# Kernel tuning notes

Measured on AMD Instinct MI355X. Metric: run time of the kernel, lower is better.

## Reference

```python
import jax, jax.numpy as jnp
import numpy as np

NUM_HEADS = 16
EMBED_DIM = 1024
HEAD_DIM = EMBED_DIM // NUM_HEADS
REG_LEN = 2048
SUM_LEN = 64
BSZ = 2
REL_DIM = 64
NUM_REL_EMB = 64
MAX_SUMMARY = 64
SCALE = HEAD_DIM ** -0.5


def _ln(x, g, b, eps=1e-5):
    m = jnp.mean(x, axis=-1, keepdims=True)
    v = jnp.mean((x - m) ** 2, axis=-1, keepdims=True)
    return (x - m) * jax.lax.rsqrt(v + eps) * g + b


def setup_inputs() -> dict:
    key = jax.random.key(0)
    ks = jax.random.split(key, 16)
    inp = {}
    inp['reg_x'] = jax.random.normal(ks[0], (REG_LEN, BSZ, EMBED_DIM), jnp.float32)
    inp['sum_token_ids'] = jax.random.randint(ks[1], (BSZ, SUM_LEN), 0, MAX_SUMMARY + 1)
    inp['rel_idx'] = jax.random.randint(ks[2], (BSZ, SUM_LEN + REG_LEN, REG_LEN), 0, NUM_REL_EMB)
    inp['sum_len'] = SUM_LEN
    inp['reg_len'] = REG_LEN
    emb = jax.random.normal(ks[3], (MAX_SUMMARY + 1, EMBED_DIM), jnp.float32) * 0.02
    inp['emb_sum'] = emb.at[0].set(0.0)  # padding_idx = 0
    inp['rel_emb0'] = jax.random.normal(ks[4], (NUM_REL_EMB, REL_DIM), jnp.float32) * 0.02

    def lin(k, din, dout):
        return jax.random.normal(k, (din, dout), jnp.float32) * (1.0 / np.sqrt(din))

    inp['Wq'] = lin(ks[5], EMBED_DIM, EMBED_DIM); inp['bq'] = jnp.zeros((EMBED_DIM,), jnp.float32)
    inp['Wk'] = lin(ks[6], EMBED_DIM, EMBED_DIM); inp['bk'] = jnp.zeros((EMBED_DIM,), jnp.float32)
    inp['Wv'] = lin(ks[7], EMBED_DIM, EMBED_DIM); inp['bv'] = jnp.zeros((EMBED_DIM,), jnp.float32)
    inp['Wr0'] = lin(ks[8], REL_DIM, EMBED_DIM); inp['br0'] = jnp.zeros((EMBED_DIM,), jnp.float32)
    inp['Wk2'] = lin(ks[9], HEAD_DIM, HEAD_DIM); inp['bk2'] = jnp.zeros((HEAD_DIM,), jnp.float32)
    inp['Wv2'] = lin(ks[10], HEAD_DIM, HEAD_DIM); inp['bv2'] = jnp.zeros((HEAD_DIM,), jnp.float32)
    inp['Wo'] = lin(ks[11], EMBED_DIM, EMBED_DIM); inp['bo'] = jnp.zeros((EMBED_DIM,), jnp.float32)
    for name in ['ln_k', 'ln_v', 'ln_k2', 'ln_v2']:
        inp[name + '_g'] = jnp.ones((HEAD_DIM,), jnp.float32)
        inp[name + '_b'] = jnp.zeros((HEAD_DIM,), jnp.float32)
    return inp


def reference(reg_x, sum_token_ids, rel_idx, sum_len, reg_len, emb_sum, rel_emb0,
              Wq, bq, Wk, bk, Wv, bv, Wr0, br0, Wk2, bk2, Wv2, bv2, Wo, bo,
              ln_k_g, ln_k_b, ln_v_g, ln_v_b, ln_k2_g, ln_k2_b, ln_v2_g, ln_v2_b):
    R, B, E = reg_x.shape  # reg_len, bsz, embed_dim
    H, D = NUM_HEADS, HEAD_DIM
    S = sum_token_ids.shape[1]

    # regular K/V projections + per-head LayerNorm
    reg_k = _ln((reg_x @ Wk + bk).reshape(R, B, H, D), ln_k_g, ln_k_b)
    reg_v = _ln((reg_x @ Wv + bv).reshape(R, B, H, D), ln_v_g, ln_v_b)

    # relation-type embedding projection -> [Rrel, H, D]
    r0 = (rel_emb0 @ Wr0 + br0).reshape(NUM_REL_EMB, H, D)

    # --- stage 1: summary tokens attend over regular tokens ---
    sum_x = emb_sum[sum_token_ids.T]                     # [S, B, E]
    sum_q = sum_x.reshape(S, B, H, D) * SCALE
    scores_sum = jnp.einsum('sbhd,kbhd->bhsk', sum_q, reg_k)   # [B,H,S,R]
    qr_sum = jnp.einsum('sbhd,Zhd->bhsZ', sum_q, r0)           # [B,H,S,Rrel]
    idx_sum = rel_idx[:, :S]                                   # [B,S,R]
    scores_sum = scores_sum + jnp.take_along_axis(qr_sum, idx_sum[:, None, :, :], axis=-1)
    w_sum = jax.nn.softmax(scores_sum, axis=-1)
    sum_x2 = jnp.einsum('bhsk,kbhd->sbhd', w_sum, reg_v)       # [S,B,H,D]

    sum_k2 = _ln(sum_x2 @ Wk2 + bk2, ln_k2_g, ln_k2_b)
    sum_v2 = _ln(sum_x2 @ Wv2 + bv2, ln_v2_g, ln_v2_b)

    # --- stage 2: regular tokens attend over [summary ; regular] keys ---
    reg_q = (reg_x @ Wq + bq).reshape(R, B, H, D) * SCALE
    scores_rs = jnp.einsum('qbhd,sbhd->bhqs', reg_q, sum_k2)   # [B,H,R,S]
    scores_rr = jnp.einsum('qbhd,kbhd->bhqk', reg_q, reg_k)    # [B,H,R,R]
    qr_reg = jnp.einsum('qbhd,Zhd->bhqZ', reg_q, r0)
    idx_reg = rel_idx[:, S:]                                   # [B,R,R]
    scores_rr = scores_rr + jnp.take_along_axis(qr_reg, idx_reg[:, None, :, :], axis=-1)
    scores = jnp.concatenate([scores_rs, scores_rr], axis=-1)  # [B,H,R,S+R]
    w = jax.nn.softmax(scores, axis=-1)
    v_all = jnp.concatenate([sum_v2, reg_v], axis=0)           # [S+R,B,H,D]
    attn_out = jnp.einsum('bhqk,kbhd->qbhd', w, v_all).reshape(R, B, E)
    reg_x2 = attn_out @ Wo + bo
    return reg_x2
```

## Files before the change

### kernel.cpp

```cpp
#include <hip/hip_runtime.h>
#include <cstdint>
#include <cstddef>

#define NH   16
#define HD   64
#define RLEN 2048
#define BSZ  2
#define SLEN 64
#define NZ   64
#define ED   1024
#define KTOT 2112
#define NSPLIT 16

#define QSCALE 0.18033688011112042f

typedef __bf16 bf16_t;
typedef bf16_t bf16x8 __attribute__((ext_vector_type(8)));
typedef bf16_t bf16x4 __attribute__((ext_vector_type(4)));
typedef float  f32x4  __attribute__((ext_vector_type(4)));

__device__ __forceinline__ f32x4 mfma16(bf16x8 a, bf16x8 b, f32x4 c) {
    return __builtin_amdgcn_mfma_f32_16x16x32_bf16(a, b, c, 0, 0, 0);
}

__device__ __forceinline__ void dma16(const void* g, void* l) {
    __builtin_amdgcn_global_load_lds(
        (const __attribute__((address_space(1))) unsigned int*)g,
        (__attribute__((address_space(3))) unsigned int*)l, 16, 0, 0);
}


template<int BM>
__global__ __launch_bounds__(256) void gemm_fast(
    const bf16_t* __restrict__ A, const bf16_t* __restrict__ Bt,
    const float* __restrict__ b0, const float* __restrict__ b1,
    const float* __restrict__ b2,
    bf16_t* __restrict__ oq, float* __restrict__ o1, float* __restrict__ o2,
    int M, int K, int N, int mode)
{
    constexpr int MT = BM / 64;
    __shared__ __align__(16) bf16_t As[BM * 64];
    __shared__ __align__(16) bf16_t Bs[128 * 64];

    const int t = threadIdx.x;
    const int wave = t >> 6, lane = t & 63;
    const int quad = lane >> 4, l15 = lane & 15;
    const int rsub = lane >> 3, gq = lane & 7;
    const int m0 = blockIdx.y * BM, n0 = blockIdx.x * 128;

    f32x4 acc[MT][8];
#pragma unroll
    for (int i = 0; i < MT; i++)
#pragma unroll
        for (int j = 0; j < 8; j++) acc[i][j] = (f32x4){0.f, 0.f, 0.f, 0.f};

    for (int k0 = 0; k0 < K; k0 += 64) {
#pragma unroll
        for (int j = 0; j < BM / 32; j++) {
            int row = wave * (BM / 4) + j * 8 + rsub;
            const bf16_t* g = A + (size_t)(m0 + row) * K + k0 + ((gq ^ (row & 7)) * 8);
            dma16(g, As + (wave * (BM / 4) + j * 8) * 64);
        }
#pragma unroll
        for (int j = 0; j < 4; j++) {
            int row = wave * 32 + j * 8 + rsub;
            const bf16_t* g = Bt + (size_t)(n0 + row) * K + k0 + ((gq ^ (row & 7)) * 8);
            dma16(g, Bs + (wave * 32 + j * 8) * 64);
        }
        __syncthreads();

#pragma unroll
        for (int kk = 0; kk < 2; kk++) {
            const int pg = ((kk * 4 + quad) ^ (l15 & 7)) * 8;
            bf16x8 af[MT], bf[8];
#pragma unroll
            for (int mt = 0; mt < MT; mt++)
                af[mt] = *(const bf16x8*)(As + (wave * (BM / 4) + mt * 16 + l15) * 64 + pg);
#pragma unroll
            for (int nt = 0; nt < 8; nt++)
                bf[nt] = *(const bf16x8*)(Bs + (nt * 16 + l15) * 64 + pg);
#pragma unroll
            for (int mt = 0; mt < MT; mt++)
#pragma unroll
                for (int nt = 0; nt < 8; nt++)
                    acc[mt][nt] = mfma16(af[mt], bf[nt], acc[mt][nt]);
        }
        __syncthreads();
    }

#pragma unroll
    for (int mt = 0; mt < MT; mt++)
#pragma unroll
        for (int nt = 0; nt < 8; nt++)
#pragma unroll
            for (int reg = 0; reg < 4; reg++) {
                int m = m0 + wave * (BM / 4) + mt * 16 + quad * 4 + reg;
                int n = n0 + nt * 16 + l15;
                if (mode == 0) {
                    o1[(size_t)m * N + n] = acc[mt][nt][reg] + b0[n];
                } else {
                    int seg = n >> 10, nl = n & 1023;
                    const float* bias = (seg == 0) ? b0 : (seg == 1) ? b1 : b2;
                    float c = acc[mt][nt][reg] + bias[nl];
                    int h = nl >> 6, d = nl & 63;
                    int r = m >> 1, bb = m & 1;
                    size_t off = (((size_t)bb * NH + h) * RLEN + r) * HD + d;
                    if (seg == 0)      oq[off] = (bf16_t)(c * QSCALE);
                    else if (seg == 1) o1[off] = c;
                    else               o2[off] = c;
                }
            }
}

__global__ __launch_bounds__(256) void gemm_mfma(
    const bf16_t* __restrict__ A, const bf16_t* __restrict__ Bt,
    const float* __restrict__ bias, float* __restrict__ outf,
    int M, int K, int N, int Rr)
{
    constexpr int LDA = 40;
    __shared__ __align__(16) bf16_t As[64 * LDA];
    __shared__ __align__(16) bf16_t Bs[128 * LDA];

    const int t = threadIdx.x;
    const int wave = t >> 6, lane = t & 63;
    const int quad = lane >> 4, l15 = lane & 15;
    const int wrow = wave >> 1, wcol = wave & 1;
    const int m0 = blockIdx.y * 64, n0 = blockIdx.x * 128;

    f32x4 acc[2][4];
#pragma unroll
    for (int i = 0; i < 2; i++)
#pragma unroll
        for (int j = 0; j < 4; j++) acc[i][j] = (f32x4){0.f, 0.f, 0.f, 0.f};

    const int srow = t >> 2, sseg = (t & 3) * 8;

    for (int k0 = 0; k0 < K; k0 += 32) {
        bf16x8 av  = *(const bf16x8*)(A  + (size_t)(m0 + srow) * K + k0 + sseg);
        bf16x8 bv0 = *(const bf16x8*)(Bt + (size_t)(n0 + srow) * K + k0 + sseg);
        bf16x8 bv1 = *(const bf16x8*)(Bt + (size_t)(n0 + 64 + srow) * K + k0 + sseg);
        __syncthreads();
        *(bf16x8*)(As + srow * LDA + sseg)        = av;
        *(bf16x8*)(Bs + srow * LDA + sseg)        = bv0;
        *(bf16x8*)(Bs + (64 + srow) * LDA + sseg) = bv1;
        __syncthreads();

        bf16x8 af[2], bf[4];
#pragma unroll
        for (int mt = 0; mt < 2; mt++)
            af[mt] = *(const bf16x8*)(As + (wrow * 32 + mt * 16 + l15) * LDA + quad * 8);
#pragma unroll
        for (int nt = 0; nt < 4; nt++)
            bf[nt] = *(const bf16x8*)(Bs + (wcol * 64 + nt * 16 + l15) * LDA + quad * 8);
#pragma unroll
        for (int mt = 0; mt < 2; mt++)
#pragma unroll
            for (int nt = 0; nt < 4; nt++)
                acc[mt][nt] = mfma16(af[mt], bf[nt], acc[mt][nt]);
    }

#pragma unroll
    for (int mt = 0; mt < 2; mt++)
#pragma unroll
        for (int nt = 0; nt < 4; nt++)
#pragma unroll
            for (int reg = 0; reg < 4; reg++) {
                int m = m0 + wrow * 32 + mt * 16 + quad * 4 + reg;
                int n = n0 + wcol * 64 + nt * 16 + l15;
                if (m >= M) continue;
                float c = acc[mt][nt][reg] + bias[n];
                int h = n >> 6, d = n & 63;
                outf[(((size_t)h) * Rr + m) * HD + d] = c;
            }
}

__global__ __launch_bounds__(256) void ln_k_frag(
    const float* __restrict__ x, const float* __restrict__ g, const float* __restrict__ b,
    bf16_t* __restrict__ kfm)
{
    int row  = blockIdx.x * 4 + (threadIdx.x >> 6);
    int lane = threadIdx.x & 63;
    float v = x[(size_t)row * HD + lane];
    float s1 = v, s2 = v * v;
#pragma unroll
    for (int o = 32; o > 0; o >>= 1) {
        s1 += __shfl_xor(s1, o);
        s2 += __shfl_xor(s2, o);
    }
    float mean = s1 * (1.f / 64.f);
    float var  = s2 * (1.f / 64.f) - mean * mean;
    float y = (v - mean) * rsqrtf(var + 1e-5f) * g[lane] + b[lane];
    int bh = row >> 11, r = row & 2047, d = lane;
    int rt = r & 63;
    size_t off = (size_t)bh * 131072 + (size_t)(r >> 6) * 4096 +
        (size_t)((((rt & 3) * 2 + (d >> 5)) * 64 + ((d >> 3) & 3) * 16 + (rt >> 2)) * 8 + (d & 7));
    kfm[off] = (bf16_t)y;
}

__global__ __launch_bounds__(256) void lnv_frag(
    const float* __restrict__ v, const float* __restrict__ g,
    const float* __restrict__ b, bf16_t* __restrict__ vfm)
{
    __shared__ float tile[64][65];
    const int bh = blockIdx.y, tidx = blockIdx.x;
    const int t = threadIdx.x;
    const int wave = t >> 6, lane = t & 63;

#pragma unroll
    for (int i = 0; i < 16; i++) {
        int rl = wave * 16 + i;
        float x = v[((size_t)bh * RLEN + tidx * 64 + rl) * HD + lane];
        float s1 = x, s2 = x * x;
#pragma unroll
        for (int o = 32; o > 0; o >>= 1) {
            s1 += __shfl_xor(s1, o);
            s2 += __shfl_xor(s2, o);
        }
        float mean = s1 * (1.f / 64.f);
        float var  = s2 * (1.f / 64.f) - mean * mean;
        tile[rl][lane] = (x - mean) * rsqrtf(var + 1e-5f) * g[lane] + b[lane];
    }
    __syncthreads();
    int d = t >> 2, rs = (t & 3) * 16;
    bf16x8 o0, o1;
#pragma unroll
    for (int j = 0; j < 8; j++) {
        o0[j] = (bf16_t)tile[rs + j][d];
        o1[j] = (bf16_t)tile[rs + 8 + j][d];
    }
    size_t base = (size_t)bh * 131072;
    size_t off0 = base + (size_t)((((tidx * 4 + (d >> 4)) * 2 + (rs >> 5)) * 64
                  + ((rs >> 3) & 3) * 16 + (d & 15)) * 8);
    int rs2 = rs + 8;
    size_t off1 = base + (size_t)((((tidx * 4 + (d >> 4)) * 2 + (rs2 >> 5)) * 64
                  + ((rs2 >> 3) & 3) * 16 + (d & 15)) * 8);
    *(bf16x8*)(vfm + off0) = o0;
    *(bf16x8*)(vfm + off1) = o1;
}

__global__ __launch_bounds__(256) void cvt_bf16(
    const float* __restrict__ src, bf16_t* __restrict__ dst, int n)
{
    int i = (blockIdx.x * 256 + threadIdx.x) * 4;
    if (i < n) {
        float4 v = *(const float4*)(src + i);
        bf16x4 o;
        o[0] = (bf16_t)v.x; o[1] = (bf16_t)v.y; o[2] = (bf16_t)v.z; o[3] = (bf16_t)v.w;
        *(bf16x4*)(dst + i) = o;
    }
}

__global__ __launch_bounds__(256) void prep_batch(
    const float* __restrict__ Wq, const float* __restrict__ Wk,
    const float* __restrict__ Wv, const float* __restrict__ Wo,
    const float* __restrict__ Wr0,
    bf16_t* __restrict__ wqt, bf16_t* __restrict__ wkt,
    bf16_t* __restrict__ wvt, bf16_t* __restrict__ wot,
    bf16_t* __restrict__ wr0t,
    const float* __restrict__ emb, const int* __restrict__ ids,
    bf16_t* __restrict__ sum_q,
    const float* __restrict__ rel_emb0, bf16_t* __restrict__ re0b)
{
    const int bid = blockIdx.x;
    const int t = threadIdx.x;

    if (bid >= 1168) {
        int i = ((bid - 1168) * 256 + t) * 4;
        float4 v = *(const float4*)(rel_emb0 + i);
        bf16x4 o;
        o[0] = (bf16_t)v.x; o[1] = (bf16_t)v.y; o[2] = (bf16_t)v.z; o[3] = (bf16_t)v.w;
        *(bf16x4*)(re0b + i) = o;
        return;
    }
    if (bid >= 1040) {
        int sb = bid - 1040;
        int s = sb >> 1, b = sb & 1;
        int id = ids[b * SLEN + s];
        const float* src = emb + (size_t)id * ED;
        for (int e = t; e < ED; e += 256) {
            int h = e >> 6, d = e & 63;
            sum_q[(((size_t)b * NH + h) * SLEN + s) * HD + d] = (bf16_t)(src[e] * QSCALE);
        }
        return;
    }

    __shared__ float tile[64][65];
    const float* src; bf16_t* dst; int R, C, r0, c0;
    if (bid < 1024) {
        int sel = bid >> 8, local = bid & 255;
        src = (sel == 0) ? Wq : (sel == 1) ? Wk : (sel == 2) ? Wv : Wo;
        dst = (sel == 0) ? wqt : (sel == 1) ? wkt : (sel == 2) ? wvt : wot;
        R = ED; C = ED; r0 = (local >> 4) * 64; c0 = (local & 15) * 64;
    } else {
        src = Wr0; dst = wr0t; R = NZ; C = ED; r0 = 0; c0 = (bid - 1024) * 64;
    }
#pragma unroll
    for (int i = 0; i < 4; i++) {
        int idx = t + i * 256;
        int r = idx >> 4, c = (idx & 15) * 4;
        float4 vv = *(const float4*)(src + (size_t)(r0 + r) * C + c0 + c);
        tile[r][c] = vv.x; tile[r][c + 1] = vv.y; tile[r][c + 2] = vv.z; tile[r][c + 3] = vv.w;
    }
    __syncthreads();
    int cc = t >> 2, rs = (t & 3) * 16;
    bf16x8 o0, o1;
#pragma unroll
    for (int j = 0; j < 8; j++) {
        o0[j] = (bf16_t)tile[rs + j][cc];
        o1[j] = (bf16_t)tile[rs + 8 + j][cc];
    }
    *(bf16x8*)(dst + (size_t)(c0 + cc) * R + r0 + rs) = o0;
    *(bf16x8*)(dst + (size_t)(c0 + cc) * R + r0 + rs + 8) = o1;
}

template<int MT>
__device__ __forceinline__ void attn_tile(
    const bf16_t* __restrict__ ktn, const bf16_t* __restrict__ vtn, int koffn,
    const int* __restrict__ relbase, bool userel,
    const float* __restrict__ qrsw, bf16_t* __restrict__ Psw,
    const bf16x8 (&qf)[MT][2],
    bf16x8 (&kf)[4][2], bf16x8 (&vf)[4][2], int4 (&crel)[MT][4],
    f32x4 (&O)[MT][4], float (&l_i)[MT][4],
    int quad, int l15, int lane)
{
    f32x4 S[MT][4];
#pragma unroll
    for (int mt = 0; mt < MT; mt++)
#pragma unroll
        for (int nt = 0; nt < 4; nt++) {
            f32x4 acc = (f32x4){0.f, 0.f, 0.f, 0.f};
            acc = mfma16(qf[mt][0], kf[nt][0], acc);
            acc = mfma16(qf[mt][1], kf[nt][1], acc);
            S[mt][nt] = acc;
        }

#pragma unroll
    for (int nt = 0; nt < 4; nt++)
#pragma unroll
        for (int kb = 0; kb < 2; kb++)
            kf[nt][kb] = *(const bf16x8*)(ktn + ((nt * 2 + kb) * 64 + lane) * 8);

    if (userel) {
#pragma unroll
        for (int mt = 0; mt < MT; mt++)
#pragma unroll
            for (int reg = 0; reg < 4; reg++) {
                const float* qr = qrsw + (mt * 16 + quad * 4 + reg) * 64;
                int4 c = crel[mt][reg];
                S[mt][0][reg] += qr[c.x];
                S[mt][1][reg] += qr[c.y];
                S[mt][2][reg] += qr[c.z];
                S[mt][3][reg] += qr[c.w];
            }
    }

#pragma unroll
    for (int mt = 0; mt < MT; mt++)
#pragma unroll
        for (int reg = 0; reg < 4; reg++)
            crel[mt][reg] = *(const int4*)(relbase + (size_t)(mt * 16 + reg) * RLEN + koffn);

#pragma unroll
    for (int mt = 0; mt < MT; mt++)
#pragma unroll
        for (int nt = 0; nt < 4; nt++)
#pragma unroll
            for (int reg = 0; reg < 4; reg++)
                S[mt][nt][reg] = exp2f(S[mt][nt][reg]);

    bf16x8 ones;
#pragma unroll
    for (int j = 0; j < 8; j++) ones[j] = (bf16_t)1.0f;

#pragma unroll
    for (int mt = 0; mt < MT; mt++)
#pragma unroll
        for (int reg = 0; reg < 4; reg++) {
            bf16x4 pv;
            pv[0] = (bf16_t)S[mt][0][reg]; pv[1] = (bf16_t)S[mt][1][reg];
            pv[2] = (bf16_t)S[mt][2][reg]; pv[3] = (bf16_t)S[mt][3][reg];
            *(bf16x4*)(Psw + (mt * 16 + quad * 4 + reg) * 72 + 4 * l15) = pv;
        }

#pragma unroll
    for (int mt = 0; mt < MT; mt++) {
        bf16x8 pf0 = *(const bf16x8*)(Psw + (mt * 16 + l15) * 72 + quad * 8);
        bf16x8 pf1 = *(const bf16x8*)(Psw + (mt * 16 + l15) * 72 + 32 + quad * 8);
        f32x4 ls = (f32x4){0.f, 0.f, 0.f, 0.f};
        ls = mfma16(pf0, ones, ls);
        ls = mfma16(pf1, ones, ls);
#pragma unroll
        for (int nt = 0; nt < 4; nt++) {
            O[mt][nt] = mfma16(pf0, vf[nt][0], O[mt][nt]);
            O[mt][nt] = mfma16(pf1, vf[nt][1], O[mt][nt]);
        }
#pragma unroll
        for (int reg = 0; reg < 4; reg++) l_i[mt][reg] += ls[reg];
    }

#pragma unroll
    for (int nt = 0; nt < 4; nt++)
#pragma unroll
        for (int kb = 0; kb < 2; kb++)
            vf[nt][kb] = *(const bf16x8*)(vtn + ((nt * 2 + kb) * 64 + lane) * 8);
}

__device__ __forceinline__ void load_kv(
    bf16x8 (&kf)[4][2], bf16x8 (&vf)[4][2],
    const bf16_t* __restrict__ kt, const bf16_t* __restrict__ vt, int lane)
{
#pragma unroll
    for (int nt = 0; nt < 4; nt++)
#pragma unroll
        for (int kb = 0; kb < 2; kb++) {
            kf[nt][kb] = *(const bf16x8*)(kt + ((nt * 2 + kb) * 64 + lane) * 8);
            vf[nt][kb] = *(const bf16x8*)(vt + ((nt * 2 + kb) * 64 + lane) * 8);
        }
}

template<int MT>
__device__ __forceinline__ void build_qr(
    const float* __restrict__ r0, int h, const bf16x8 (&qf)[MT][2],
    float* __restrict__ qrsw, int quad, int l15)
{
#pragma unroll
    for (int nt = 0; nt < 4; nt++) {
        const float* rp = r0 + ((size_t)h * NZ + l15 + 16 * nt) * HD + quad * 8;
        float4 a0 = *(const float4*)(rp);
        float4 a1 = *(const float4*)(rp + 4);
        bf16x8 bf0;
        bf0[0] = (bf16_t)a0.x; bf0[1] = (bf16_t)a0.y; bf0[2] = (bf16_t)a0.z; bf0[3] = (bf16_t)a0.w;
        bf0[4] = (bf16_t)a1.x; bf0[5] = (bf16_t)a1.y; bf0[6] = (bf16_t)a1.z; bf0[7] = (bf16_t)a1.w;
        float4 b0 = *(const float4*)(rp + 32);
        float4 b1 = *(const float4*)(rp + 36);
        bf16x8 bf1;
        bf1[0] = (bf16_t)b0.x; bf1[1] = (bf16_t)b0.y; bf1[2] = (bf16_t)b0.z; bf1[3] = (bf16_t)b0.w;
        bf1[4] = (bf16_t)b1.x; bf1[5] = (bf16_t)b1.y; bf1[6] = (bf16_t)b1.z; bf1[7] = (bf16_t)b1.w;
#pragma unroll
        for (int mt = 0; mt < MT; mt++) {
            f32x4 qa = (f32x4){0.f, 0.f, 0.f, 0.f};
            qa = mfma16(qf[mt][0], bf0, qa);
            qa = mfma16(qf[mt][1], bf1, qa);
#pragma unroll
            for (int reg = 0; reg < 4; reg++)
                qrsw[(mt * 16 + quad * 4 + reg) * 64 + l15 + 16 * nt] = qa[reg];
        }
    }
}

__global__ __launch_bounds__(256) void sum_attn_split(
    const bf16_t* __restrict__ Qb,
    const bf16_t* __restrict__ kfm, const bf16_t* __restrict__ vfm,
    const float*  __restrict__ r0,
    const int*    __restrict__ rel_idx,
    float* __restrict__ po, float* __restrict__ pl)
{
    constexpr int TPS = 32 / NSPLIT;
    const int bh = blockIdx.x;
    const int split = blockIdx.y;
    const int b = bh >> 4, h = bh & 15;
    const int t = threadIdx.x;
    const int wave = t >> 6, lane = t & 63;
    const int quad = lane >> 4, l15 = lane & 15;

    __shared__ __align__(16) bf16_t Ps[4][16 * 72];
    __shared__ float qrs[4][16 * 64];

    bf16x8 qf[1][2];
    const bf16_t* Qrow = Qb + ((size_t)bh * SLEN + wave * 16 + l15) * HD;
    qf[0][0] = *(const bf16x8*)(Qrow + quad * 8);
    qf[0][1] = *(const bf16x8*)(Qrow + 32 + quad * 8);

    const int* relbase = rel_idx + ((size_t)b * KTOT + wave * 16 + quad * 4) * RLEN + 4 * l15;
    const bf16_t* kbase = kfm + (size_t)bh * 131072 + (size_t)(split * TPS) * 4096;
    const bf16_t* vbase = vfm + (size_t)bh * 131072 + (size_t)(split * TPS) * 4096;

    bf16x8 kf[4][2], vf[4][2];
    int4 crel[1][4];
    load_kv(kf, vf, kbase, vbase, lane);
#pragma unroll
    for (int reg = 0; reg < 4; reg++)
        crel[0][reg] = *(const int4*)(relbase + (size_t)reg * RLEN + split * TPS * 64);

    build_qr<1>(r0, h, qf, qrs[wave], quad, l15);

    f32x4 O[1][4];
    float l_i[1][4];
#pragma unroll
    for (int nt = 0; nt < 4; nt++) O[0][nt] = (f32x4){0.f, 0.f, 0.f, 0.f};
#pragma unroll
    for (int r = 0; r < 4; r++) l_i[0][r] = 0.f;

    for (int i = 0; i < TPS; i++) {
        const int nx = (i < TPS - 1) ? i + 1 : i;
        attn_tile<1>(kbase + (size_t)nx * 4096, vbase + (size_t)nx * 4096,
                     (split * TPS + nx) * 64, relbase, true,
                     qrs[wave], Ps[wave], qf, kf, vf, crel,
                     O, l_i, quad, l15, lane);
    }

    const size_t pslot = (size_t)bh * NSPLIT + split;
#pragma unroll
    for (int nt = 0; nt < 4; nt++)
#pragma unroll
        for (int reg = 0; reg < 4; reg++) {
            int sq = wave * 16 + quad * 4 + reg;
            po[(pslot * SLEN + sq) * HD + l15 + 16 * nt] = O[0][nt][reg];
        }
#pragma unroll
    for (int reg = 0; reg < 4; reg++) {
        int sq = wave * 16 + quad * 4 + reg;
        if (l15 == 0) pl[pslot * SLEN + sq] = l_i[0][reg];
    }
}

__global__ __launch_bounds__(64) void k2v2_fused(
    const float* __restrict__ po, const float* __restrict__ pl,
    const float* __restrict__ Wk2, const float* __restrict__ bk2,
    const float* __restrict__ Wv2, const float* __restrict__ bv2,
    const float* __restrict__ gk, const float* __restrict__ bk,
    const float* __restrict__ gv, const float* __restrict__ bv,
    bf16_t* __restrict__ k2fm, bf16_t* __restrict__ v2fm)
{
    int row = blockIdx.x;
    int d = threadIdx.x;
    int bh = row >> 6, s = row & 63;

    float L = 0.f, acc = 0.f;
#pragma unroll
    for (int j = 0; j < NSPLIT; j++) {
        L += pl[((size_t)bh * NSPLIT + j) * SLEN + s];
        acc += po[(((size_t)bh * NSPLIT + j) * SLEN + s) * HD + d];
    }
    __shared__ float xs[64];
    xs[d] = acc / L;
    __syncthreads();

#pragma unroll
    for (int which = 0; which < 2; which++) {
        const float* W  = which ? Wv2 : Wk2;
        const float* bi = which ? bv2 : bk2;
        const float* g  = which ? gv : gk;
        const float* bb = which ? bv : bk;
        float a = bi[d];
#pragma unroll
        for (int j = 0; j < 64; j++) a += xs[j] * W[j * HD + d];
        float s1 = a, s2 = a * a;
#pragma unroll
        for (int o = 32; o > 0; o >>= 1) {
            s1 += __shfl_xor(s1, o);
            s2 += __shfl_xor(s2, o);
        }
        float mean = s1 * (1.f / 64.f);
        float var  = s2 * (1.f / 64.f) - mean * mean;
        float y = (a - mean) * rsqrtf(var + 1e-5f) * g[d] + bb[d];
        if (which == 0) {
            size_t off = (size_t)bh * 4096 +
                (size_t)((((s & 3) * 2 + (d >> 5)) * 64
                          + ((d >> 3) & 3) * 16 + (s >> 2)) * 8 + (d & 7));
            k2fm[off] = (bf16_t)y;
        } else {
            size_t off = (size_t)bh * 4096 +
                (size_t)((((d >> 4) * 2 + (s >> 5)) * 64
                          + ((s >> 3) & 3) * 16 + (d & 15)) * 8 + (s & 7));
            v2fm[off] = (bf16_t)y;
        }
    }
}

__global__ __launch_bounds__(256) void reg_attn_mfma(
    const bf16_t* __restrict__ Qb,
    const bf16_t* __restrict__ kfm, const bf16_t* __restrict__ vfm,
    const bf16_t* __restrict__ k2fm, const bf16_t* __restrict__ v2fm,
    const float*  __restrict__ r0,
    const int*    __restrict__ rel_idx,
    bf16_t* __restrict__ attn_out)
{
    const int bid = blockIdx.x;
    const int bh = (bid & 7) * 4 + ((bid >> 3) & 3);
    const int qt = bid >> 5;
    const int b = bh >> 4, h = bh & 15;
    const int q0 = qt * 128;

    const int t = threadIdx.x;
    const int wave = t >> 6, lane = t & 63;
    const int quad = lane >> 4, l15 = lane & 15;

    __shared__ __align__(16) bf16_t Ps[4][32 * 72];
    __shared__ float qrs[4][32 * 64];

    bf16x8 qf[2][2];
#pragma unroll
    for (int mt = 0; mt < 2; mt++) {
        const bf16_t* Qrow = Qb + ((size_t)bh * RLEN + q0 + wave * 32 + mt * 16 + l15) * HD;
        qf[mt][0] = *(const bf16x8*)(Qrow + quad * 8);
        qf[mt][1] = *(const bf16x8*)(Qrow + 32 + quad * 8);
    }

    bf16x8 kf[4][2], vf[4][2];
    int4 crel[2][4];
    load_kv(kf, vf, k2fm + (size_t)bh * 4096, v2fm + (size_t)bh * 4096, lane);

    build_qr<2>(r0, h, qf, qrs[wave], quad, l15);

    f32x4 O[2][4];
    float l_i[2][4];
#pragma unroll
    for (int mt = 0; mt < 2; mt++)
#pragma unroll
        for (int nt = 0; nt < 4; nt++) O[mt][nt] = (f32x4){0.f, 0.f, 0.f, 0.f};
#pragma unroll
    for (int mt = 0; mt < 2; mt++)
#pragma unroll
        for (int r = 0; r < 4; r++) l_i[mt][r] = 0.f;

    const int* relbase = rel_idx +
        ((size_t)b * KTOT + SLEN + q0 + wave * 32 + quad * 4) * RLEN + 4 * l15;

    const bf16_t* kt = kfm + (size_t)bh * 131072;
    const bf16_t* vt = vfm + (size_t)bh * 131072;

    attn_tile<2>(kt, vt, 0, relbase, false, qrs[wave], Ps[wave], qf,
                 kf, vf, crel, O, l_i, quad, l15, lane);

    for (int tile = 0; tile < 32; tile++) {
        const int nx = (tile < 31) ? tile + 1 : tile;
        attn_tile<2>(kt + (size_t)nx * 4096, vt + (size_t)nx * 4096, nx * 64,
                     relbase, true, qrs[wave], Ps[wave], qf,
                     kf, vf, crel, O, l_i, quad, l15, lane);
    }

#pragma unroll
    for (int mt = 0; mt < 2; mt++) {
        float linv[4];
#pragma unroll
        for (int reg = 0; reg < 4; reg++) linv[reg] = 1.0f / l_i[mt][reg];
#pragma unroll
        for (int nt = 0; nt < 4; nt++)
#pragma unroll
            for (int reg = 0; reg < 4; reg++) {
                int q = q0 + wave * 32 + mt * 16 + quad * 4 + reg;
                attn_out[((size_t)q * BSZ + b) * ED + h * HD + l15 + 16 * nt] =
                    (bf16_t)(O[mt][nt][reg] * linv[reg]);
            }
    }
}

extern "C" void kernel_launch(void* const* d_in, const int* in_sizes, int n_in,
                              void* d_out, int out_size, void* d_ws, size_t ws_size,
                              hipStream_t stream)
{
    const float* reg_x    = (const float*)d_in[0];
    const int*   sum_ids  = (const int*)d_in[1];
    const int*   rel_idx  = (const int*)d_in[2];
    const float* emb_sum  = (const float*)d_in[5];
    const float* rel_emb0 = (const float*)d_in[6];
    const float* Wq = (const float*)d_in[7];
    const float* bq = (const float*)d_in[8];
    const float* Wk = (const float*)d_in[9];
    const float* bk = (const float*)d_in[10];
    const float* Wv = (const float*)d_in[11];
    const float* bv = (const float*)d_in[12];
    const float* Wr0 = (const float*)d_in[13];
    const float* br0 = (const float*)d_in[14];
    const float* Wk2 = (const float*)d_in[15];
    const float* bk2 = (const float*)d_in[16];
    const float* Wv2 = (const float*)d_in[17];
    const float* bv2 = (const float*)d_in[18];
    const float* Wo  = (const float*)d_in[19];
    const float* bo  = (const float*)d_in[20];
    const float* ln_k_g  = (const float*)d_in[21];
    const float* ln_k_b  = (const float*)d_in[22];
    const float* ln_v_g  = (const float*)d_in[23];
    const float* ln_v_b  = (const float*)d_in[24];
    const float* ln_k2_g = (const float*)d_in[25];
    const float* ln_k2_b = (const float*)d_in[26];
    const float* ln_v2_g = (const float*)d_in[27];
    const float* ln_v2_b = (const float*)d_in[28];

    const size_t QKV = (size_t)BSZ * NH * RLEN * HD;
    const size_t SUM = (size_t)BSZ * NH * SLEN * HD;

    float* ws  = (float*)d_ws;
    float* k   = ws;
    float* v   = k + QKV;
    float* r0  = v + QKV;

    bf16_t* xb   = (bf16_t*)(r0 + (size_t)NH * NZ * HD);
    bf16_t* qb   = xb + QKV;
    bf16_t* kfm  = qb + QKV;
    bf16_t* vfm  = kfm + QKV;
    bf16_t* sqb  = vfm + QKV;
    bf16_t* k2fm = sqb + SUM;
    bf16_t* v2fm = k2fm + SUM;
    bf16_t* wqt  = v2fm + SUM;
    bf16_t* wkt  = wqt + (size_t)ED * ED;
    bf16_t* wvt  = wkt + (size_t)ED * ED;
    bf16_t* wot  = wvt + (size_t)ED * ED;
    bf16_t* wr0t = wot + (size_t)ED * ED;
    bf16_t* re0b = wr0t + (size_t)ED * NZ;
    bf16_t* aob  = (bf16_t*)k;
    float*  po   = v;
    float*  pl   = po + (size_t)BSZ * NH * NSPLIT * SLEN * HD;

    const int M = RLEN * BSZ;

    cvt_bf16<<<(int)(QKV / 1024), 256, 0, stream>>>(reg_x, xb, (int)QKV);
    prep_batch<<<1172, 256, 0, stream>>>(Wq, Wk, Wv, Wo, Wr0,
                                         wqt, wkt, wvt, wot, wr0t,
                                         emb_sum, sum_ids, sqb, rel_emb0, re0b);

    gemm_fast<128><<<dim3(3 * ED / 128, M / 128), 256, 0, stream>>>(
        xb, wqt, bq, bk, bv, qb, k, v, M, ED, 3 * ED, 1);

    ln_k_frag<<<(BSZ * NH * RLEN) / 4, 256, 0, stream>>>(k, ln_k_g, ln_k_b, kfm);
    lnv_frag<<<dim3(RLEN / 64, BSZ * NH), 256, 0, stream>>>(v, ln_v_g, ln_v_b, vfm);

    gemm_mfma<<<dim3(ED / 128, 1), 256, 0, stream>>>(re0b, wr0t, br0, r0, NZ, NZ, ED, NZ);

    sum_attn_split<<<dim3(BSZ * NH, NSPLIT), 256, 0, stream>>>(sqb, kfm, vfm, r0, rel_idx, po, pl);

    k2v2_fused<<<BSZ * NH * SLEN, 64, 0, stream>>>(po, pl, Wk2, bk2, Wv2, bv2,
                                                   ln_k2_g, ln_k2_b, ln_v2_g, ln_v2_b,
                                                   k2fm, v2fm);

    reg_attn_mfma<<<512, 256, 0, stream>>>(qb, kfm, vfm, k2fm, v2fm, r0, rel_idx, aob);

    gemm_fast<64><<<dim3(ED / 128, M / 64), 256, 0, stream>>>(
        aob, wot, bo, nullptr, nullptr, nullptr, (float*)d_out, nullptr, M, ED, ED, 0);
}
```

Before: 370.7 us.

## Fuse K/V LayerNorm and fragment layout into QKV GEMM epilogue

```diff
diff --git a/kernel.cpp b/kernel.cpp
--- a/kernel.cpp
+++ b/kernel.cpp
@@ -35,12 +35,16 @@
     const bf16_t* __restrict__ A, const bf16_t* __restrict__ Bt,
     const float* __restrict__ b0, const float* __restrict__ b1,
     const float* __restrict__ b2,
-    bf16_t* __restrict__ oq, float* __restrict__ o1, float* __restrict__ o2,
+    const float* __restrict__ gk_, const float* __restrict__ bk_,
+    const float* __restrict__ gv_, const float* __restrict__ bv_,
+    bf16_t* __restrict__ oq, float* __restrict__ o1,
+    bf16_t* __restrict__ okf, bf16_t* __restrict__ ovf,
     int M, int K, int N, int mode)
 {
     constexpr int MT = BM / 64;
     __shared__ __align__(16) bf16_t As[BM * 64];
     __shared__ __align__(16) bf16_t Bs[128 * 64];
+    __shared__ __align__(16) bf16_t trs[64][66];
 
     const int t = threadIdx.x;
     const int wave = t >> 6, lane = t & 63;
@@ -88,28 +92,137 @@
         __syncthreads();
     }
 
-#pragma unroll
-    for (int mt = 0; mt < MT; mt++)
-#pragma unroll
-        for (int nt = 0; nt < 8; nt++)
+    if (mode == 0) {
+#pragma unroll
+        for (int mt = 0; mt < MT; mt++)
+#pragma unroll
+            for (int nt = 0; nt < 8; nt++)
+#pragma unroll
+                for (int reg = 0; reg < 4; reg++) {
+                    int m = m0 + wave * (BM / 4) + mt * 16 + quad * 4 + reg;
+                    int n = n0 + nt * 16 + l15;
+                    o1[(size_t)m * N + n] = acc[mt][nt][reg] + b0[n];
+                }
+        return;
+    }
+
+    const int seg = n0 >> 10;
+    if (seg == 0) {
+#pragma unroll
+        for (int mt = 0; mt < MT; mt++)
+#pragma unroll
+            for (int nt = 0; nt < 8; nt++)
+#pragma unroll
+                for (int reg = 0; reg < 4; reg++) {
+                    int m = m0 + wave * (BM / 4) + mt * 16 + quad * 4 + reg;
+                    int n = n0 + nt * 16 + l15;
+                    float c = acc[mt][nt][reg] + b0[n];
+                    int h = n >> 6, d = n & 63;
+                    int r = m >> 1, bb2 = m & 1;
+                    size_t off = (((size_t)bb2 * NH + h) * RLEN + r) * HD + d;
+                    oq[off] = (bf16_t)(c * QSCALE);
+                }
+        return;
+    }
+
+    const int nl0 = n0 & 1023, h0 = nl0 >> 6;
+    const float* bias = (seg == 1) ? b1 : b2;
+    const float* lg = (seg == 1) ? gk_ : gv_;
+    const float* lb = (seg == 1) ? bk_ : bv_;
+    float gj[4], bj[4], bsv[2][4];
+#pragma unroll
+    for (int j = 0; j < 4; j++) { gj[j] = lg[j * 16 + l15]; bj[j] = lb[j * 16 + l15]; }
+#pragma unroll
+    for (int h2 = 0; h2 < 2; h2++)
+#pragma unroll
+        for (int j = 0; j < 4; j++)
+            bsv[h2][j] = bias[nl0 + (h2 * 4 + j) * 16 + l15];
+
+    if (seg == 1) {
+#pragma unroll
+        for (int mt = 0; mt < MT; mt++)
 #pragma unroll
             for (int reg = 0; reg < 4; reg++) {
                 int m = m0 + wave * (BM / 4) + mt * 16 + quad * 4 + reg;
-                int n = n0 + nt * 16 + l15;
-                if (mode == 0) {
-                    o1[(size_t)m * N + n] = acc[mt][nt][reg] + b0[n];
-                } else {
-                    int seg = n >> 10, nl = n & 1023;
-                    const float* bias = (seg == 0) ? b0 : (seg == 1) ? b1 : b2;
-                    float c = acc[mt][nt][reg] + bias[nl];
-                    int h = nl >> 6, d = nl & 63;
-                    int r = m >> 1, bb = m & 1;
-                    size_t off = (((size_t)bb * NH + h) * RLEN + r) * HD + d;
-                    if (seg == 0)      oq[off] = (bf16_t)(c * QSCALE);
-                    else if (seg == 1) o1[off] = c;
-                    else               o2[off] = c;
+                int r = m >> 1, bb2 = m & 1, rt = r & 63;
+#pragma unroll
+                for (int h2 = 0; h2 < 2; h2++) {
+                    float c[4], s1 = 0.f, s2 = 0.f;
+#pragma unroll
+                    for (int j = 0; j < 4; j++) {
+                        c[j] = acc[mt][h2 * 4 + j][reg] + bsv[h2][j];
+                        s1 += c[j]; s2 += c[j] * c[j];
+                    }
+#pragma unroll
+                    for (int o = 1; o < 16; o <<= 1) {
+                        s1 += __shfl_xor(s1, o);
+                        s2 += __shfl_xor(s2, o);
+                    }
+                    float mean = s1 * (1.f / 64.f);
+                    float rsi = rsqrtf(s2 * (1.f / 64.f) - mean * mean + 1e-5f);
+                    size_t base = (size_t)(bb2 * NH + h0 + h2) * 131072
+                                + (size_t)(r >> 6) * 4096;
+#pragma unroll
+                    for (int j = 0; j < 4; j++) {
+                        int d = j * 16 + l15;
+                        float y = (c[j] - mean) * rsi * gj[j] + bj[j];
+                        okf[base + (size_t)((((rt & 3) * 2 + (d >> 5)) * 64
+                              + ((d >> 3) & 3) * 16 + (rt >> 2)) * 8 + (d & 7))] = (bf16_t)y;
+                    }
                 }
             }
+    } else {
+        const int tidx = m0 >> 7;
+        const int dd = t >> 2, rs2 = (t & 3) * 16;
+#pragma unroll
+        for (int pb = 0; pb < 2; pb++)
+#pragma unroll
+            for (int h2 = 0; h2 < 2; h2++) {
+#pragma unroll
+                for (int mt = 0; mt < MT; mt++)
+#pragma unroll
+                    for (int rsel = 0; rsel < 2; rsel++) {
+                        const int reg = pb + 2 * rsel;
+                        const int key = wave * (BM / 8) + mt * 8 + quad * 2 + rsel;
+                        float c[4], s1 = 0.f, s2 = 0.f;
+#pragma unroll
+                        for (int j = 0; j < 4; j++) {
+                            c[j] = acc[mt][h2 * 4 + j][reg] + bsv[h2][j];
+                            s1 += c[j]; s2 += c[j] * c[j];
+                        }
+#pragma unroll
+                        for (int o = 1; o < 16; o <<= 1) {
+                            s1 += __shfl_xor(s1, o);
+                            s2 += __shfl_xor(s2, o);
+                        }
+                        float mean = s1 * (1.f / 64.f);
+                        float rsi = rsqrtf(s2 * (1.f / 64.f) - mean * mean + 1e-5f);
+#pragma unroll
+                        for (int j = 0; j < 4; j++) {
+                            float y = (c[j] - mean) * rsi * gj[j] + bj[j];
+                            trs[key][j * 16 + l15] = (bf16_t)y;
+                        }
+                    }
+                __syncthreads();
+                {
+                    bf16x8 o0v, o1v;
+#pragma unroll
+                    for (int j = 0; j < 8; j++) {
+                        o0v[j] = trs[rs2 + j][dd];
+                        o1v[j] = trs[rs2 + 8 + j][dd];
+                    }
+                    size_t base = (size_t)(pb * NH + h0 + h2) * 131072;
+                    size_t off0 = base + (size_t)((((tidx * 4 + (dd >> 4)) * 2 + (rs2 >> 5)) * 64
+                                  + ((rs2 >> 3) & 3) * 16 + (dd & 15)) * 8);
+                    int rsb = rs2 + 8;
+                    size_t off1 = base + (size_t)((((tidx * 4 + (dd >> 4)) * 2 + (rsb >> 5)) * 64
+                                  + ((rsb >> 3) & 3) * 16 + (dd & 15)) * 8);
+                    *(bf16x8*)(ovf + off0) = o0v;
+                    *(bf16x8*)(ovf + off1) = o1v;
+                }
+                __syncthreads();
+            }
+    }
 }
 
 __global__ __launch_bounds__(256) void gemm_mfma(
@@ -174,83 +287,8 @@
             }
 }
 
-__global__ __launch_bounds__(256) void ln_k_frag(
-    const float* __restrict__ x, const float* __restrict__ g, const float* __restrict__ b,
-    bf16_t* __restrict__ kfm)
-{
-    int row  = blockIdx.x * 4 + (threadIdx.x >> 6);
-    int lane = threadIdx.x & 63;
-    float v = x[(size_t)row * HD + lane];
-    float s1 = v, s2 = v * v;
-#pragma unroll
-    for (int o = 32; o > 0; o >>= 1) {
-        s1 += __shfl_xor(s1, o);
-        s2 += __shfl_xor(s2, o);
-    }
-    float mean = s1 * (1.f / 64.f);
-    float var  = s2 * (1.f / 64.f) - mean * mean;
-    float y = (v - mean) * rsqrtf(var + 1e-5f) * g[lane] + b[lane];
-    int bh = row >> 11, r = row & 2047, d = lane;
-    int rt = r & 63;
-    size_t off = (size_t)bh * 131072 + (size_t)(r >> 6) * 4096 +
-        (size_t)((((rt & 3) * 2 + (d >> 5)) * 64 + ((d >> 3) & 3) * 16 + (rt >> 2)) * 8 + (d & 7));
-    kfm[off] = (bf16_t)y;
-}
-
-__global__ __launch_bounds__(256) void lnv_frag(
-    const float* __restrict__ v, const float* __restrict__ g,
-    const float* __restrict__ b, bf16_t* __restrict__ vfm)
-{
-    __shared__ float tile[64][65];
-    const int bh = blockIdx.y, tidx = blockIdx.x;
-    const int t = threadIdx.x;
-    const int wave = t >> 6, lane = t & 63;
-
-#pragma unroll
-    for (int i = 0; i < 16; i++) {
-        int rl = wave * 16 + i;
-        float x = v[((size_t)bh * RLEN + tidx * 64 + rl) * HD + lane];
-        float s1 = x, s2 = x * x;
-#pragma unroll
-        for (int o = 32; o > 0; o >>= 1) {
-            s1 += __shfl_xor(s1, o);
-            s2 += __shfl_xor(s2, o);
-        }
-        float mean = s1 * (1.f / 64.f);
-        float var  = s2 * (1.f / 64.f) - mean * mean;
-        tile[rl][lane] = (x - mean) * rsqrtf(var + 1e-5f) * g[lane] + b[lane];
-    }
-    __syncthreads();
-    int d = t >> 2, rs = (t & 3) * 16;
-    bf16x8 o0, o1;
-#pragma unroll
-    for (int j = 0; j < 8; j++) {
-        o0[j] = (bf16_t)tile[rs + j][d];
-        o1[j] = (bf16_t)tile[rs + 8 + j][d];
-    }
-    size_t base = (size_t)bh * 131072;
-    size_t off0 = base + (size_t)((((tidx * 4 + (d >> 4)) * 2 + (rs >> 5)) * 64
-                  + ((rs >> 3) & 3) * 16 + (d & 15)) * 8);
-    int rs2 = rs + 8;
-    size_t off1 = base + (size_t)((((tidx * 4 + (d >> 4)) * 2 + (rs2 >> 5)) * 64
-                  + ((rs2 >> 3) & 3) * 16 + (d & 15)) * 8);
-    *(bf16x8*)(vfm + off0) = o0;
-    *(bf16x8*)(vfm + off1) = o1;
-}
-
-__global__ __launch_bounds__(256) void cvt_bf16(
-    const float* __restrict__ src, bf16_t* __restrict__ dst, int n)
-{
-    int i = (blockIdx.x * 256 + threadIdx.x) * 4;
-    if (i < n) {
-        float4 v = *(const float4*)(src + i);
-        bf16x4 o;
-        o[0] = (bf16_t)v.x; o[1] = (bf16_t)v.y; o[2] = (bf16_t)v.z; o[3] = (bf16_t)v.w;
-        *(bf16x4*)(dst + i) = o;
-    }
-}
-
 __global__ __launch_bounds__(256) void prep_batch(
+    const float* __restrict__ regx, bf16_t* __restrict__ xb,
     const float* __restrict__ Wq, const float* __restrict__ Wk,
     const float* __restrict__ Wv, const float* __restrict__ Wo,
     const float* __restrict__ Wr0,
@@ -261,8 +299,16 @@
     bf16_t* __restrict__ sum_q,
     const float* __restrict__ rel_emb0, bf16_t* __restrict__ re0b)
 {
-    const int bid = blockIdx.x;
     const int t = threadIdx.x;
+    if (blockIdx.x < 4096) {
+        int i = (blockIdx.x * 256 + t) * 4;
+        float4 v = *(const float4*)(regx + i);
+        bf16x4 o;
+        o[0] = (bf16_t)v.x; o[1] = (bf16_t)v.y; o[2] = (bf16_t)v.z; o[3] = (bf16_t)v.w;
+        *(bf16x4*)(xb + i) = o;
+        return;
+    }
+    const int bid = blockIdx.x - 4096;
 
     if (bid >= 1168) {
         int i = ((bid - 1168) * 256 + t) * 4;
@@ -681,11 +727,7 @@
     const size_t QKV = (size_t)BSZ * NH * RLEN * HD;
     const size_t SUM = (size_t)BSZ * NH * SLEN * HD;
 
-    float* ws  = (float*)d_ws;
-    float* k   = ws;
-    float* v   = k + QKV;
-    float* r0  = v + QKV;
-
+    float*  r0   = (float*)d_ws;
     bf16_t* xb   = (bf16_t*)(r0 + (size_t)NH * NZ * HD);
     bf16_t* qb   = xb + QKV;
     bf16_t* kfm  = qb + QKV;
@@ -699,22 +741,20 @@
     bf16_t* wot  = wvt + (size_t)ED * ED;
     bf16_t* wr0t = wot + (size_t)ED * ED;
     bf16_t* re0b = wr0t + (size_t)ED * NZ;
-    bf16_t* aob  = (bf16_t*)k;
-    float*  po   = v;
+    float*  po   = (float*)(re0b + (size_t)NZ * 64);
     float*  pl   = po + (size_t)BSZ * NH * NSPLIT * SLEN * HD;
+    bf16_t* aob  = (bf16_t*)po;
 
     const int M = RLEN * BSZ;
 
-    cvt_bf16<<<(int)(QKV / 1024), 256, 0, stream>>>(reg_x, xb, (int)QKV);
-    prep_batch<<<1172, 256, 0, stream>>>(Wq, Wk, Wv, Wo, Wr0,
-                                         wqt, wkt, wvt, wot, wr0t,
-                                         emb_sum, sum_ids, sqb, rel_emb0, re0b);
+    prep_batch<<<4096 + 1172, 256, 0, stream>>>(
+        reg_x, xb, Wq, Wk, Wv, Wo, Wr0,
+        wqt, wkt, wvt, wot, wr0t,
+        emb_sum, sum_ids, sqb, rel_emb0, re0b);
 
     gemm_fast<128><<<dim3(3 * ED / 128, M / 128), 256, 0, stream>>>(
-        xb, wqt, bq, bk, bv, qb, k, v, M, ED, 3 * ED, 1);
-
-    ln_k_frag<<<(BSZ * NH * RLEN) / 4, 256, 0, stream>>>(k, ln_k_g, ln_k_b, kfm);
-    lnv_frag<<<dim3(RLEN / 64, BSZ * NH), 256, 0, stream>>>(v, ln_v_g, ln_v_b, vfm);
+        xb, wqt, bq, bk, bv, ln_k_g, ln_k_b, ln_v_g, ln_v_b,
+        qb, nullptr, kfm, vfm, M, ED, 3 * ED, 1);
 
     gemm_mfma<<<dim3(ED / 128, 1), 256, 0, stream>>>(re0b, wr0t, br0, r0, NZ, NZ, ED, NZ);
 
@@ -727,5 +767,6 @@
     reg_attn_mfma<<<512, 256, 0, stream>>>(qb, kfm, vfm, k2fm, v2fm, r0, rel_idx, aob);
 
     gemm_fast<64><<<dim3(ED / 128, M / 64), 256, 0, stream>>>(
-        aob, wot, bo, nullptr, nullptr, nullptr, (float*)d_out, nullptr, M, ED, ED, 0);
-}
+        aob, wot, bo, nullptr, nullptr, nullptr, nullptr, nullptr, nullptr,
+        nullptr, (float*)d_out, nullptr, nullptr, M, ED, ED, 0);
+}
```

Result: faster. 344.6 us (-7.1%).
